# Kernel tuning notes

Measured on AMD Instinct MI355X. Metric: run time of the kernel, lower is better.

Reference implementation:

```python
import jax, jax.numpy as jnp
import numpy as np

B, T, C, H, D = 2, 2048, 1024, 16, 64


def setup_inputs() -> dict:
    key = jax.random.key(0)
    k1, k2, k3, k4, k5 = jax.random.split(key, 5)
    x = jax.random.normal(k1, (B, T, C), dtype=jnp.float32)
    Wq = jax.random.normal(k2, (H, C, D), dtype=jnp.float32) * 0.02
    Wk = jax.random.normal(k3, (H, C, D), dtype=jnp.float32) * 0.02
    Wv = jax.random.normal(k4, (H, C, D), dtype=jnp.float32) * 0.02
    Wo = jax.random.normal(k5, (C, C), dtype=jnp.float32) * 0.02
    bo = jnp.zeros((C,), dtype=jnp.float32)
    return {"x": x, "Wq": Wq, "Wk": Wk, "Wv": Wv, "Wo": Wo, "bo": bo}


def reference(x, Wq, Wk, Wv, Wo, bo):
    # per-head projections (batched over heads instead of a python loop)
    q = jnp.einsum('btc,hcd->bhtd', x, Wq)
    k = jnp.einsum('btc,hcd->bhtd', x, Wk)
    v = jnp.einsum('btc,hcd->bhtd', x, Wv)
    scale = jnp.asarray(D, x.dtype) ** -0.5
    wei = jnp.einsum('bhtd,bhsd->bhts', q, k) * scale  # [B,H,T,T]
    causal = jnp.tril(jnp.ones((T, T), dtype=bool))
    wei = jnp.where(causal, wei, jnp.asarray(-jnp.inf, wei.dtype))
    attn = jax.nn.softmax(wei, axis=-1)
    out = jnp.einsum('bhts,bhsd->bhtd', attn, v)  # [B,H,T,D]
    # concat heads (head order h0..hH-1 along feature dim)
    out = out.transpose(0, 2, 1, 3).reshape(B, T, C)
    # output projection: nn.Linear -> y = x @ W^T + b  (dropout p=0 is identity)
    return out @ Wo.T + bo
```

## Files before the change

### kernel.cpp

```cpp
#include <hip/hip_runtime.h>
#include <hip/hip_bf16.h>
#include <cstdint>
#include <math.h>

#define B_DIM 2
#define T_SEQ 2048
#define C_DIM 1024
#define H_NUM 16
#define D_HEAD 64
#define M_ROWS (B_DIM * T_SEQ)
#define N_QKV (3 * H_NUM * D_HEAD)

using short8  = __attribute__((ext_vector_type(8))) short;
using short4v = __attribute__((ext_vector_type(4))) short;
using f32x4   = __attribute__((ext_vector_type(4))) float;

__device__ __forceinline__ short f2bf(float f) {
  union { __hip_bfloat16 h; short s; } u;
  u.h = __float2bfloat16(f);
  return u.s;
}

__device__ __forceinline__ unsigned pk2bf(float a, float b) {
  union { float f; unsigned u; } ua, ub;
  ua.f = a; ub.f = b;
  return __builtin_amdgcn_perm(ub.u, ua.u, 0x07060302u);
}

__device__ __forceinline__ void gld_lds16(short* lds, const short* g) {
  __builtin_amdgcn_global_load_lds(
      (const unsigned int __attribute__((address_space(1)))*)g,
      (unsigned int __attribute__((address_space(3)))*)lds, 16, 0, 0);
}

#define BAR_VM(N)                                                    \
  do {                                                               \
    asm volatile("s_waitcnt vmcnt(" #N ") lgkmcnt(0)" ::: "memory"); \
    __builtin_amdgcn_s_barrier();                                    \
    __builtin_amdgcn_sched_barrier(0);                               \
  } while (0)

__global__ __launch_bounds__(256) void prep(const float* __restrict__ x,
                                            const float* __restrict__ Wo,
                                            const float* __restrict__ Wq,
                                            const float* __restrict__ Wk,
                                            const float* __restrict__ Wv,
                                            short* __restrict__ xb,
                                            short* __restrict__ Wob,
                                            short* __restrict__ Wt) {
  int bid = blockIdx.x;
  int tid = threadIdx.x;
  if (bid < 2560) {
    const float* in = (bid < 2048) ? x : Wo;
    short* out      = (bid < 2048) ? xb : Wob;
    int i = ((bid < 2048) ? bid : (bid - 2048)) * 256 + tid;
    const float4* p = reinterpret_cast<const float4*>(in) + (size_t)i * 2;
    float4 a = p[0], b = p[1];
    short8 o;
    o[0] = f2bf(a.x); o[1] = f2bf(a.y); o[2] = f2bf(a.z); o[3] = f2bf(a.w);
    o[4] = f2bf(b.x); o[5] = f2bf(b.y); o[6] = f2bf(b.z); o[7] = f2bf(b.w);
    reinterpret_cast<short8*>(out)[i] = o;
    return;
  }
  int pid  = bid - 2560;
  int proj = pid >> 8;
  int h    = (pid >> 4) & 15;
  int cb   = pid & 15;
  const float* W = (proj == 0) ? Wq : ((proj == 1) ? Wk : Wv);
  const float* src = W + ((size_t)h * C_DIM + (size_t)cb * 64) * D_HEAD;

  __shared__ float tile[64][65];
#pragma unroll
  for (int j = 0; j < 4; j++) {
    int flat = tid + j * 256;
    int c    = flat >> 4;
    int d4   = flat & 15;
    float4 v = reinterpret_cast<const float4*>(src + (size_t)c * D_HEAD)[d4];
    tile[c][d4 * 4 + 0] = v.x;
    tile[c][d4 * 4 + 1] = v.y;
    tile[c][d4 * 4 + 2] = v.z;
    tile[c][d4 * 4 + 3] = v.w;
  }
  __syncthreads();

  int d     = tid >> 2;
  int cpart = (tid & 3) * 16;
  short* dst = Wt + ((size_t)(proj * H_NUM + h) * D_HEAD + d) * C_DIM + cb * 64 + cpart;
  short8 o0, o1;
#pragma unroll
  for (int j = 0; j < 8; j++) {
    o0[j] = f2bf(tile[cpart + j][d]);
    o1[j] = f2bf(tile[cpart + 8 + j][d]);
  }
  *reinterpret_cast<short8*>(dst)     = o0;
  *reinterpret_cast<short8*>(dst + 8) = o1;
}

template <int MODE, int BMT>
__global__ __launch_bounds__(256) void gemm_bt(
    const short* __restrict__ A, const short* __restrict__ Bt,
    const float* __restrict__ bias,
    short* __restrict__ qb, short* __restrict__ kb, short* __restrict__ vtb,
    float* __restrict__ outb,
    int M, int N, int K) {
  constexpr int BK = 32;
  constexpr int MR = BMT / 32;
  constexpr int NLA = BMT / 64;
  __shared__ short GL[3 * (BMT + 128) * BK];
  short* Asb = GL;
  short* Bsb = GL + 3 * BMT * BK;

  int tid  = threadIdx.x;
  int lane = tid & 63;
  int wv   = tid >> 6;
  int q15  = lane & 15, g = lane >> 4;
  int ntn  = N >> 7;
  int bpx  = (M / BMT) >> 3;
  int xcd  = blockIdx.x & 7;
  int idx  = blockIdx.x >> 3;
  int bn   = idx / bpx;
  int bm   = xcd * bpx + (idx - bn * bpx);
  int row0 = bm * BMT, col0 = bn << 7;
  int wm   = (wv >> 1) * (BMT / 2);
  int wn   = (wv & 1) << 6;

  f32x4 acc[MR][4];
#pragma unroll
  for (int i = 0; i < MR; i++)
#pragma unroll
    for (int j = 0; j < 4; j++) acc[i][j] = (f32x4){0.f, 0.f, 0.f, 0.f};

  int srccol = ((tid & 3) ^ ((tid >> 3) & 3)) * 8;
  const short* ag = A  + (size_t)(row0 + (tid >> 2)) * K + srccol;
  const short* bg = Bt + (size_t)(col0 + (tid >> 2)) * K + srccol;
  const size_t gstep = (size_t)64 * K;

  auto stage = [&](int ks, int buf) {
    const short* a  = ag + (size_t)ks * BK;
    const short* bb = bg + (size_t)ks * BK;
    gld_lds16(Asb + buf * BMT * BK + tid * 8, a);
    if constexpr (NLA == 2)
      gld_lds16(Asb + buf * BMT * BK + 64 * BK + tid * 8, a + gstep);
    gld_lds16(Bsb + buf * 128 * BK + tid * 8, bb);
    gld_lds16(Bsb + buf * 128 * BK + 64 * BK + tid * 8, bb + gstep);
  };

  int nk = K / BK;
  stage(0, 0);
  stage(1, 1);
  if constexpr (NLA == 2) {
    asm volatile("s_waitcnt vmcnt(4)" ::: "memory");
  } else {
    asm volatile("s_waitcnt vmcnt(3)" ::: "memory");
  }
  __builtin_amdgcn_s_barrier();
  __builtin_amdgcn_sched_barrier(0);

  int rpos = (g ^ ((q15 >> 1) & 3)) * 8;

  for (int k = 0; k < nk; ++k) {
    int buf = k % 3;
    if (k + 2 < nk) stage(k + 2, (k + 2) % 3);

    short8 af[MR], bf[4];
#pragma unroll
    for (int mi = 0; mi < MR; mi++)
      af[mi] = *reinterpret_cast<const short8*>(
          &Asb[buf * BMT * BK + (wm + mi * 16 + q15) * BK + rpos]);
#pragma unroll
    for (int ni = 0; ni < 4; ni++)
      bf[ni] = *reinterpret_cast<const short8*>(
          &Bsb[buf * 128 * BK + (wn + ni * 16 + q15) * BK + rpos]);
#pragma unroll
    for (int mi = 0; mi < MR; mi++)
#pragma unroll
      for (int ni = 0; ni < 4; ni++)
        acc[mi][ni] = __builtin_amdgcn_mfma_f32_16x16x32_bf16(af[mi], bf[ni],
                                                              acc[mi][ni], 0, 0, 0);

    if (k + 1 < nk) {
      if (k + 2 < nk) {
        if constexpr (NLA == 2) { BAR_VM(4); } else { BAR_VM(3); }
      } else {
        BAR_VM(0);
      }
    }
  }

  if constexpr (MODE == 0) {
    constexpr int LDT = 136;
    int proj  = col0 >> 10;
    int b     = row0 >> 11;
    int trow0 = row0 & (T_SEQ - 1);
    int h0    = (col0 >> 6) & 15;
    __syncthreads();
    if (proj < 2) {
      float scl = (proj == 0) ? 0.125f * 1.44269504f : 1.0f;
#pragma unroll
      for (int mi = 0; mi < MR; mi++)
#pragma unroll
        for (int ni = 0; ni < 4; ni++) {
          int t0 = wm + mi * 16 + (g << 2);
          int d2 = wn + ni * 16 + q15;
#pragma unroll
          for (int r = 0; r < 4; r++)
            GL[(t0 + r) * LDT + d2] = f2bf(acc[mi][ni][r] * scl);
        }
      __syncthreads();
      short* dstb = (proj == 0) ? qb : kb;
#pragma unroll
      for (int ps = 0; ps < 8; ps++) {
        int trow  = ps * 16 + (tid >> 4);
        int chunk = tid & 15;
        int hh    = h0 + (chunk >> 3);
        int d     = (chunk & 7) * 8;
        short8 v = *reinterpret_cast<const short8*>(&GL[trow * LDT + chunk * 8]);
        *reinterpret_cast<short8*>(
            dstb + ((size_t)(b * H_NUM + hh) * T_SEQ + trow0 + trow) * D_HEAD + d) = v;
      }
    } else {
#pragma unroll
      for (int mi = 0; mi < MR; mi++)
#pragma unroll
        for (int ni = 0; ni < 4; ni++) {
          int t0 = wm + mi * 16 + (g << 2);
          int d2 = wn + ni * 16 + q15;
          short4v pk;
#pragma unroll
          for (int r = 0; r < 4; r++) pk[r] = f2bf(acc[mi][ni][r]);
          *reinterpret_cast<short4v*>(&GL[d2 * LDT + t0]) = pk;
        }
      __syncthreads();
#pragma unroll
      for (int ps = 0; ps < 8; ps++) {
        int drow  = ps * 16 + (tid >> 4);
        int chunk = tid & 15;
        int hh    = h0 + (drow >> 6);
        int d     = drow & 63;
        short8 v = *reinterpret_cast<const short8*>(&GL[drow * LDT + chunk * 8]);
        *reinterpret_cast<short8*>(
            vtb + ((size_t)(b * H_NUM + hh) * D_HEAD + d) * T_SEQ + trow0 +
            chunk * 8) = v;
      }
    }
  } else {
#pragma unroll
    for (int mi = 0; mi < MR; mi++) {
#pragma unroll
      for (int ni = 0; ni < 4; ni++) {
        int rb  = row0 + wm + mi * 16 + (g << 2);
        int col = col0 + wn + ni * 16 + q15;
        f32x4 v = acc[mi][ni];
        float bb = bias[col];
#pragma unroll
        for (int r = 0; r < 4; r++)
          outb[(size_t)(rb + r) * N + col] = v[r] + bb;
      }
    }
  }
}

__global__ __launch_bounds__(256, 4) void attn_fwd(const short* __restrict__ qg,
                                                   const short* __restrict__ kg,
                                                   const short* __restrict__ vt,
                                                   short* __restrict__ ob) {
  int bid  = blockIdx.x;
  int q2   = bid >> 8;
  int r    = bid & 255;
  int bh   = (r & 7) * 4 + q2;
  int sb   = r >> 3;
  int strip = (q2 & 1) ? sb : 31 - sb;
  int b    = bh >> 4;
  int h    = bh & 15;
  int tid  = threadIdx.x, lane = tid & 63, wv = tid >> 6;
  int q15  = lane & 15, g = lane >> 4;
  int qr   = strip * 64 + wv * 16;

  __shared__ short arena[16384];

  const short* qp = qg + (size_t)bh * T_SEQ * D_HEAD;
  const short* kp = kg + (size_t)bh * T_SEQ * D_HEAD;
  const short* vp = vt + (size_t)bh * D_HEAD * T_SEQ;

  int r8    = lane >> 3;
  int gcb   = ((lane & 7) * 16) ^ (r8 << 4);
  int srow0 = wv * 16;

  int hh = (q15 & 7) << 4;
  int koff0 = ((0 * 64 + g * 16) ^ hh) >> 1;
  int koff1 = ((1 * 64 + g * 16) ^ hh) >> 1;
  int voff[4];
#pragma unroll
  for (int st = 0; st < 4; st++) voff[st] = ((st * 32 + g * 8) ^ hh) >> 1;

  short8 qf[2];
#pragma unroll
  for (int kk = 0; kk < 2; kk++)
    qf[kk] = *reinterpret_cast<const short8*>(
        qp + (size_t)(qr + q15) * D_HEAD + kk * 32 + g * 8);

  f32x4 acc[4];
#pragma unroll
  for (int dt = 0; dt < 4; dt++) acc[dt] = (f32x4){0.f, 0.f, 0.f, 0.f};
  f32x4 lacc = (f32x4){0.f, 0.f, 0.f, 0.f};
  float m_ = -1e30f;

  const short4v ones4 = (short4v){(short)0x3F80, (short)0x3F80,
                                  (short)0x3F80, (short)0x3F80};

  int nch = strip + 1;

  auto stage = [&](int c, int pbuf) {
    const short* ks = kp + (size_t)(c * 64 + srow0 + r8) * D_HEAD + (gcb >> 1);
    const short* vs = vp + (size_t)(srow0 + r8) * T_SEQ + c * 64 + (gcb >> 1);
    short* kd = arena + pbuf * 4096 + srow0 * 64 + lane * 8;
    short* vd = arena + 8192 + pbuf * 4096 + srow0 * 64 + lane * 8;
    gld_lds16(kd, ks);
    gld_lds16(kd + 8 * 64, ks + (size_t)8 * D_HEAD);
    gld_lds16(vd, vs);
    gld_lds16(vd + 8 * 64, vs + (size_t)8 * T_SEQ);
  };

  stage(0, 0);
  BAR_VM(0);

  for (int c = 0; c < nch; ++c) {
    int s0 = c * 64;
    if (c + 1 < nch) stage(c + 1, (c + 1) & 1);
    const short* Kb = arena + (c & 1) * 4096;
    const short* Vb = arena + 8192 + (c & 1) * 4096;

    short8 kf[4][2];
#pragma unroll
    for (int st = 0; st < 4; st++) {
      int rbase = (st * 16 + q15) * 64;
      kf[st][0] = *reinterpret_cast<const short8*>(&Kb[rbase + koff0]);
      kf[st][1] = *reinterpret_cast<const short8*>(&Kb[rbase + koff1]);
    }

    f32x4 sv[4];
#pragma unroll
    for (int st = 0; st < 4; st++) {
      f32x4 s = (f32x4){0.f, 0.f, 0.f, 0.f};
      s = __builtin_amdgcn_mfma_f32_16x16x32_bf16(kf[st][0], qf[0], s, 0, 0, 0);
      s = __builtin_amdgcn_mfma_f32_16x16x32_bf16(kf[st][1], qf[1], s, 0, 0, 0);
      sv[st] = s;
    }

    short4v vf[4][4];
#pragma unroll
    for (int st = 0; st < 4; st++)
#pragma unroll
      for (int dt = 0; dt < 4; dt++)
        vf[st][dt] = *reinterpret_cast<const short4v*>(
            &Vb[(dt * 16 + q15) * 64 + voff[st]]);

    if (c == nch - 1) {
#pragma unroll
      for (int st = 0; st < 4; st++)
#pragma unroll
        for (int r2 = 0; r2 < 4; r2++) {
          int sg = s0 + st * 16 + g * 4 + r2;
          if (sg > qr + q15) sv[st][r2] = -1e30f;
        }
    }

    float t0 = fmaxf(fmaxf(sv[0][0], sv[0][1]), sv[0][2]);
    float t1 = fmaxf(fmaxf(sv[0][3], sv[1][0]), sv[1][1]);
    float t2 = fmaxf(fmaxf(sv[1][2], sv[1][3]), sv[2][0]);
    float t3 = fmaxf(fmaxf(sv[2][1], sv[2][2]), sv[2][3]);
    float t4 = fmaxf(fmaxf(sv[3][0], sv[3][1]), sv[3][2]);
    float mx = fmaxf(fmaxf(fmaxf(t0, t1), t2),
                     fmaxf(fmaxf(t3, t4), sv[3][3]));
    mx = fmaxf(mx, __shfl_xor(mx, 16));
    mx = fmaxf(mx, __shfl_xor(mx, 32));

    if (!__all(mx <= m_ + 11.5f)) {
      float mnew = fmaxf(m_, mx);
      float sc   = __builtin_amdgcn_exp2f(m_ - mnew);
      m_ = mnew;
      lacc *= sc;
#pragma unroll
      for (int dt = 0; dt < 4; dt++) acc[dt] *= sc;
    }
    float mcur = m_;

    short4v pbf[4];
#pragma unroll
    for (int st = 0; st < 4; st++) {
      float p0 = __builtin_amdgcn_exp2f(sv[st][0] - mcur);
      float p1 = __builtin_amdgcn_exp2f(sv[st][1] - mcur);
      float p2 = __builtin_amdgcn_exp2f(sv[st][2] - mcur);
      float p3 = __builtin_amdgcn_exp2f(sv[st][3] - mcur);
      union { short4v s; unsigned u[2]; } P;
      P.u[0] = pk2bf(p0, p1);
      P.u[1] = pk2bf(p2, p3);
      pbf[st] = P.s;
    }

#pragma unroll
    for (int st = 0; st < 4; st++) {
#if __has_builtin(__builtin_amdgcn_mfma_f32_16x16x16bf16_1k)
      lacc = __builtin_amdgcn_mfma_f32_16x16x16bf16_1k(ones4, pbf[st], lacc, 0, 0, 0);
#pragma unroll
      for (int dt = 0; dt < 4; dt++)
        acc[dt] = __builtin_amdgcn_mfma_f32_16x16x16bf16_1k(
            vf[st][dt], pbf[st], acc[dt], 0, 0, 0);
#else
      short4v p4 = pbf[st];
      short8 bz = (short8){p4[0], p4[1], p4[2], p4[3], 0, 0, 0, 0};
      short8 oz = (short8){(short)0x3F80, (short)0x3F80, (short)0x3F80,
                           (short)0x3F80, 0, 0, 0, 0};
      lacc = __builtin_amdgcn_mfma_f32_16x16x32_bf16(oz, bz, lacc, 0, 0, 0);
#pragma unroll
      for (int dt = 0; dt < 4; dt++) {
        short4v v4 = vf[st][dt];
        short8 az = (short8){v4[0], v4[1], v4[2], v4[3], 0, 0, 0, 0};
        acc[dt] =
            __builtin_amdgcn_mfma_f32_16x16x32_bf16(az, bz, acc[dt], 0, 0, 0);
      }
#endif
    }

    BAR_VM(0);
  }

  short* OlW = arena + wv * (16 * 68);
  float inv = 1.0f / lacc[0];
#pragma unroll
  for (int dt = 0; dt < 4; dt++)
#pragma unroll
    for (int r2 = 0; r2 < 4; r2++)
      OlW[q15 * 68 + dt * 16 + g * 4 + r2] = f2bf(acc[dt][r2] * inv);
  int row = lane >> 2, cb = (lane & 3) * 16;
  size_t base = ((size_t)(b * T_SEQ) + qr + row) * C_DIM + h * 64 + cb;
  const short* src = OlW + row * 68 + cb;
  *reinterpret_cast<short8*>(ob + base) = *reinterpret_cast<const short8*>(src);
  *reinterpret_cast<short8*>(ob + base + 8) =
      *reinterpret_cast<const short8*>(src + 8);
}

extern "C" void kernel_launch(void* const* d_in, const int* in_sizes, int n_in,
                              void* d_out, int out_size, void* d_ws, size_t ws_size,
                              hipStream_t stream) {
  const float* x  = (const float*)d_in[0];
  const float* Wq = (const float*)d_in[1];
  const float* Wk = (const float*)d_in[2];
  const float* Wv = (const float*)d_in[3];
  const float* Wo = (const float*)d_in[4];
  const float* bo = (const float*)d_in[5];
  float* out = (float*)d_out;

  char* ws = (char*)d_ws;
  short* xb   = (short*)(ws + 0);
  short* Wt   = (short*)(ws + 8388608);
  short* Wob  = (short*)(ws + 14680064);
  short* qb   = (short*)(ws + 16777216);
  short* kb   = (short*)(ws + 25165824);
  short* vtb  = (short*)(ws + 33554432);
  short* obuf = xb;

  prep<<<3328, 256, 0, stream>>>(x, Wo, Wq, Wk, Wv, xb, Wob, Wt);

  gemm_bt<0, 128><<<(M_ROWS / 128) * (N_QKV / 128), 256, 0, stream>>>(
      xb, Wt, nullptr, qb, kb, vtb, nullptr, M_ROWS, N_QKV, C_DIM);

  attn_fwd<<<1024, 256, 0, stream>>>(qb, kb, vtb, obuf);

  gemm_bt<1, 64><<<(M_ROWS / 64) * (C_DIM / 128), 256, 0, stream>>>(
      obuf, Wob, bo, nullptr, nullptr, nullptr, out, M_ROWS, C_DIM, C_DIM);
}
```

Baseline: 101.7 us.

## Shrink QKV GEMM tile to 64 rows and switch to double-buffered LDS pipeline

Halves the M tile of the QKV projection GEMM, doubling the block count, and replaces the three-stage LDS ring with two buffers that wait for all loads each iteration. The epilogue is generalized to arbitrary BMT with a separately sized shared buffer for the Q/K and V transposes. The goal is more parallelism and occupancy through less LDS per block. In exchange, each block reuses less data per tile and the deeper prefetch is lost, so global load latency may be exposed.

Result: slower. 112.0 us (+10.2%).

```diff
diff --git a/kernel.cpp b/kernel.cpp
--- a/kernel.cpp
+++ b/kernel.cpp
@@ -103,12 +103,15 @@
     short* __restrict__ qb, short* __restrict__ kb, short* __restrict__ vtb,
     float* __restrict__ outb,
     int M, int N, int K) {
-  constexpr int BK = 32;
-  constexpr int MR = BMT / 32;
+  constexpr int BK  = 32;
+  constexpr int MR  = BMT / 32;
   constexpr int NLA = BMT / 64;
-  __shared__ short GL[3 * (BMT + 128) * BK];
-  short* Asb = GL;
-  short* Bsb = GL + 3 * BMT * BK;
+  constexpr int STG = (BMT + 128) * BK;
+  constexpr int EPQ = BMT * 136;
+  constexpr int EPV = 128 * (BMT + 8);
+  constexpr int GL2 = (2 * STG > EPQ) ? (2 * STG) : EPQ;
+  constexpr int GLSZ = (GL2 > EPV) ? GL2 : EPV;
+  __shared__ short GL[GLSZ];
 
   int tid  = threadIdx.x;
   int lane = tid & 63;
@@ -136,59 +139,50 @@
   const size_t gstep = (size_t)64 * K;
 
   auto stage = [&](int ks, int buf) {
+    short* base = GL + buf * STG;
     const short* a  = ag + (size_t)ks * BK;
     const short* bb = bg + (size_t)ks * BK;
-    gld_lds16(Asb + buf * BMT * BK + tid * 8, a);
+    gld_lds16(base + tid * 8, a);
     if constexpr (NLA == 2)
-      gld_lds16(Asb + buf * BMT * BK + 64 * BK + tid * 8, a + gstep);
-    gld_lds16(Bsb + buf * 128 * BK + tid * 8, bb);
-    gld_lds16(Bsb + buf * 128 * BK + 64 * BK + tid * 8, bb + gstep);
+      gld_lds16(base + 64 * BK + tid * 8, a + gstep);
+    gld_lds16(base + BMT * BK + tid * 8, bb);
+    gld_lds16(base + BMT * BK + 64 * BK + tid * 8, bb + gstep);
   };
 
   int nk = K / BK;
   stage(0, 0);
-  stage(1, 1);
-  if constexpr (NLA == 2) {
-    asm volatile("s_waitcnt vmcnt(4)" ::: "memory");
-  } else {
-    asm volatile("s_waitcnt vmcnt(3)" ::: "memory");
-  }
-  __builtin_amdgcn_s_barrier();
-  __builtin_amdgcn_sched_barrier(0);
+  BAR_VM(0);
 
   int rpos = (g ^ ((q15 >> 1) & 3)) * 8;
 
   for (int k = 0; k < nk; ++k) {
-    int buf = k % 3;
-    if (k + 2 < nk) stage(k + 2, (k + 2) % 3);
+    if (k + 1 < nk) stage(k + 1, (k + 1) & 1);
+    const short* Ab = GL + (k & 1) * STG;
+    const short* Bb = Ab + BMT * BK;
 
     short8 af[MR], bf[4];
 #pragma unroll
     for (int mi = 0; mi < MR; mi++)
       af[mi] = *reinterpret_cast<const short8*>(
-          &Asb[buf * BMT * BK + (wm + mi * 16 + q15) * BK + rpos]);
+          &Ab[(wm + mi * 16 + q15) * BK + rpos]);
 #pragma unroll
     for (int ni = 0; ni < 4; ni++)
       bf[ni] = *reinterpret_cast<const short8*>(
-          &Bsb[buf * 128 * BK + (wn + ni * 16 + q15) * BK + rpos]);
+          &Bb[(wn + ni * 16 + q15) * BK + rpos]);
 #pragma unroll
     for (int mi = 0; mi < MR; mi++)
 #pragma unroll
       for (int ni = 0; ni < 4; ni++)
         acc[mi][ni] = __builtin_amdgcn_mfma_f32_16x16x32_bf16(af[mi], bf[ni],
                                                               acc[mi][ni], 0, 0, 0);
-
-    if (k + 1 < nk) {
-      if (k + 2 < nk) {
-        if constexpr (NLA == 2) { BAR_VM(4); } else { BAR_VM(3); }
-      } else {
-        BAR_VM(0);
-      }
-    }
+    BAR_VM(0);
   }
 
   if constexpr (MODE == 0) {
-    constexpr int LDT = 136;
+    constexpr int LDTQ = 136;
+    constexpr int LDTV = BMT + 8;
+    constexpr int NPS  = BMT / 16;
+    constexpr int CPR  = BMT / 8;
     int proj  = col0 >> 10;
     int b     = row0 >> 11;
     int trow0 = row0 & (T_SEQ - 1);
@@ -204,17 +198,17 @@
           int d2 = wn + ni * 16 + q15;
 #pragma unroll
           for (int r = 0; r < 4; r++)
-            GL[(t0 + r) * LDT + d2] = f2bf(acc[mi][ni][r] * scl);
+            GL[(t0 + r) * LDTQ + d2] = f2bf(acc[mi][ni][r] * scl);
         }
       __syncthreads();
       short* dstb = (proj == 0) ? qb : kb;
 #pragma unroll
-      for (int ps = 0; ps < 8; ps++) {
+      for (int ps = 0; ps < NPS; ps++) {
         int trow  = ps * 16 + (tid >> 4);
         int chunk = tid & 15;
         int hh    = h0 + (chunk >> 3);
         int d     = (chunk & 7) * 8;
-        short8 v = *reinterpret_cast<const short8*>(&GL[trow * LDT + chunk * 8]);
+        short8 v = *reinterpret_cast<const short8*>(&GL[trow * LDTQ + chunk * 8]);
         *reinterpret_cast<short8*>(
             dstb + ((size_t)(b * H_NUM + hh) * T_SEQ + trow0 + trow) * D_HEAD + d) = v;
       }
@@ -228,19 +222,20 @@
           short4v pk;
 #pragma unroll
           for (int r = 0; r < 4; r++) pk[r] = f2bf(acc[mi][ni][r]);
-          *reinterpret_cast<short4v*>(&GL[d2 * LDT + t0]) = pk;
+          *reinterpret_cast<short4v*>(&GL[d2 * LDTV + t0]) = pk;
         }
       __syncthreads();
 #pragma unroll
-      for (int ps = 0; ps < 8; ps++) {
-        int drow  = ps * 16 + (tid >> 4);
-        int chunk = tid & 15;
+      for (int ps = 0; ps < NPS; ps++) {
+        int id2   = ps * 256 + tid;
+        int drow  = id2 / CPR;
+        int ch    = id2 % CPR;
         int hh    = h0 + (drow >> 6);
         int d     = drow & 63;
-        short8 v = *reinterpret_cast<const short8*>(&GL[drow * LDT + chunk * 8]);
+        short8 v = *reinterpret_cast<const short8*>(&GL[drow * LDTV + ch * 8]);
         *reinterpret_cast<short8*>(
             vtb + ((size_t)(b * H_NUM + hh) * D_HEAD + d) * T_SEQ + trow0 +
-            chunk * 8) = v;
+            ch * 8) = v;
       }
     }
   } else {
@@ -462,7 +457,7 @@
 
   prep<<<3328, 256, 0, stream>>>(x, Wo, Wq, Wk, Wv, xb, Wob, Wt);
 
-  gemm_bt<0, 128><<<(M_ROWS / 128) * (N_QKV / 128), 256, 0, stream>>>(
+  gemm_bt<0, 64><<<(M_ROWS / 64) * (N_QKV / 128), 256, 0, stream>>>(
       xb, Wt, nullptr, qb, kb, vtb, nullptr, M_ROWS, N_QKV, C_DIM);
 
   attn_fwd<<<1024, 256, 0, stream>>>(qb, kb, vtb, obuf);
```

## Split long causal attention strips into two KV halves with a combine kernel

Applied to the files above, without the earlier changes.

Splits the 11 longest query strips (21-31) of each head into two KV-range partial blocks, which removes the causal work imbalance. Work units are reordered so heavy blocks are scheduled early. The partial outputs are stored unnormalized in bf16 along with the row max and sum. A new combine kernel merges them with a log-sum-exp rescale. This adds an extra launch, partial-buffer traffic and a small bf16 rounding on the partials, in exchange for a shorter tail and better CU balance.

After: 102.5 us. Within noise of the previous version (+0.8%).

```diff
diff --git a/kernel.cpp b/kernel.cpp
--- a/kernel.cpp
+++ b/kernel.cpp
@@ -19,6 +19,11 @@
   union { __hip_bfloat16 h; short s; } u;
   u.h = __float2bfloat16(f);
   return u.s;
+}
+__device__ __forceinline__ float bf2f(short s) {
+  union { unsigned u; float f; } v;
+  v.u = ((unsigned)(unsigned short)s) << 16;
+  return v.f;
 }
 
 __device__ __forceinline__ unsigned pk2bf(float a, float b) {
@@ -263,13 +268,18 @@
 __global__ __launch_bounds__(256, 4) void attn_fwd(const short* __restrict__ qg,
                                                    const short* __restrict__ kg,
                                                    const short* __restrict__ vt,
-                                                   short* __restrict__ ob) {
+                                                   short* __restrict__ ob,
+                                                   short* __restrict__ Pp,
+                                                   float* __restrict__ mlp) {
   int bid  = blockIdx.x;
-  int q2   = bid >> 8;
-  int r    = bid & 255;
-  int bh   = (r & 7) * 4 + q2;
-  int sb   = r >> 3;
-  int strip = (q2 & 1) ? sb : 31 - sb;
+  int bh   = (bid & 7) * 4 + ((bid >> 3) & 3);
+  int slot = bid >> 5;
+  int strip, c0, c1, half = 0;
+  bool part;
+  if (slot < 5)       { strip = 20 - slot;  c0 = 0;  c1 = strip + 1; part = false; }
+  else if (slot < 16) { strip = slot + 16;  c0 = 0;  c1 = 16;        part = true;  half = 0; }
+  else if (slot < 27) { strip = 47 - slot;  c0 = 16; c1 = strip + 1; part = true;  half = 1; }
+  else                { strip = 42 - slot;  c0 = 0;  c1 = strip + 1; part = false; }
   int b    = bh >> 4;
   int h    = bh & 15;
   int tid  = threadIdx.x, lane = tid & 63, wv = tid >> 6;
@@ -307,8 +317,6 @@
 
   const short4v ones4 = (short4v){(short)0x3F80, (short)0x3F80,
                                   (short)0x3F80, (short)0x3F80};
-
-  int nch = strip + 1;
 
   auto stage = [&](int c, int pbuf) {
     const short* ks = kp + (size_t)(c * 64 + srow0 + r8) * D_HEAD + (gcb >> 1);
@@ -321,12 +329,12 @@
     gld_lds16(vd + 8 * 64, vs + (size_t)8 * T_SEQ);
   };
 
-  stage(0, 0);
+  stage(c0, c0 & 1);
   BAR_VM(0);
 
-  for (int c = 0; c < nch; ++c) {
+  for (int c = c0; c < c1; ++c) {
     int s0 = c * 64;
-    if (c + 1 < nch) stage(c + 1, (c + 1) & 1);
+    if (c + 1 < c1) stage(c + 1, (c + 1) & 1);
     const short* Kb = arena + (c & 1) * 4096;
     const short* Vb = arena + 8192 + (c & 1) * 4096;
 
@@ -355,7 +363,7 @@
         vf[st][dt] = *reinterpret_cast<const short4v*>(
             &Vb[(dt * 16 + q15) * 64 + voff[st]]);
 
-    if (c == nch - 1) {
+    if (c == strip) {
 #pragma unroll
       for (int st = 0; st < 4; st++)
 #pragma unroll
@@ -426,18 +434,78 @@
   }
 
   short* OlW = arena + wv * (16 * 68);
-  float inv = 1.0f / lacc[0];
-#pragma unroll
-  for (int dt = 0; dt < 4; dt++)
-#pragma unroll
-    for (int r2 = 0; r2 < 4; r2++)
-      OlW[q15 * 68 + dt * 16 + g * 4 + r2] = f2bf(acc[dt][r2] * inv);
-  int row = lane >> 2, cb = (lane & 3) * 16;
-  size_t base = ((size_t)(b * T_SEQ) + qr + row) * C_DIM + h * 64 + cb;
-  const short* src = OlW + row * 68 + cb;
-  *reinterpret_cast<short8*>(ob + base) = *reinterpret_cast<const short8*>(src);
-  *reinterpret_cast<short8*>(ob + base + 8) =
-      *reinterpret_cast<const short8*>(src + 8);
+  if (!part) {
+    float inv = 1.0f / lacc[0];
+#pragma unroll
+    for (int dt = 0; dt < 4; dt++)
+#pragma unroll
+      for (int r2 = 0; r2 < 4; r2++)
+        OlW[q15 * 68 + dt * 16 + g * 4 + r2] = f2bf(acc[dt][r2] * inv);
+    int row = lane >> 2, cb = (lane & 3) * 16;
+    size_t base = ((size_t)(b * T_SEQ) + qr + row) * C_DIM + h * 64 + cb;
+    const short* src = OlW + row * 68 + cb;
+    *reinterpret_cast<short8*>(ob + base) = *reinterpret_cast<const short8*>(src);
+    *reinterpret_cast<short8*>(ob + base + 8) =
+        *reinterpret_cast<const short8*>(src + 8);
+  } else {
+#pragma unroll
+    for (int dt = 0; dt < 4; dt++)
+#pragma unroll
+      for (int r2 = 0; r2 < 4; r2++)
+        OlW[q15 * 68 + dt * 16 + g * 4 + r2] = f2bf(acc[dt][r2]);
+    int si = strip - 21;
+    int row = lane >> 2, cb = (lane & 3) * 16;
+    size_t pbase = ((size_t)(bh * 11 + si) * 2 + half) * 4096 +
+                   (wv * 16 + row) * 64 + cb;
+    const short* src = OlW + row * 68 + cb;
+    *reinterpret_cast<short8*>(Pp + pbase) =
+        *reinterpret_cast<const short8*>(src);
+    *reinterpret_cast<short8*>(Pp + pbase + 8) =
+        *reinterpret_cast<const short8*>(src + 8);
+    if (lane < 16) {
+      float* mlr = mlp + ((size_t)((bh * 11 + si) * 2 + half)) * 128 +
+                   (wv * 16 + lane) * 2;
+      mlr[0] = m_;
+      mlr[1] = lacc[0];
+    }
+  }
+}
+
+__global__ __launch_bounds__(256) void combine(const short* __restrict__ Pp,
+                                               const float* __restrict__ mlp,
+                                               short* __restrict__ ob) {
+  int bid = blockIdx.x;
+  int bh  = bid / 11, si = bid % 11;
+  int strip = si + 21;
+  int b = bh >> 4, h = bh & 15;
+  int t = threadIdx.x;
+  int lr = t >> 2, dg = (t & 3) * 16;
+
+  size_t mbase = ((size_t)(bh * 11 + si) * 2) * 128 + lr * 2;
+  float m0 = mlp[mbase], l0 = mlp[mbase + 1];
+  float m1 = mlp[mbase + 128], l1 = mlp[mbase + 129];
+  float m  = fmaxf(m0, m1);
+  float w0 = __builtin_amdgcn_exp2f(m0 - m);
+  float w1 = __builtin_amdgcn_exp2f(m1 - m);
+  float inv = 1.0f / (l0 * w0 + l1 * w1);
+  w0 *= inv;
+  w1 *= inv;
+
+  const short* P0 = Pp + ((size_t)(bh * 11 + si) * 2) * 4096 + lr * 64 + dg;
+  const short* P1 = P0 + 4096;
+  short8 a0 = *reinterpret_cast<const short8*>(P0);
+  short8 a1 = *reinterpret_cast<const short8*>(P0 + 8);
+  short8 c0 = *reinterpret_cast<const short8*>(P1);
+  short8 c1 = *reinterpret_cast<const short8*>(P1 + 8);
+  short8 o0, o1;
+#pragma unroll
+  for (int j = 0; j < 8; j++) {
+    o0[j] = f2bf(bf2f(a0[j]) * w0 + bf2f(c0[j]) * w1);
+    o1[j] = f2bf(bf2f(a1[j]) * w0 + bf2f(c1[j]) * w1);
+  }
+  short* dst = ob + ((size_t)(b * T_SEQ) + strip * 64 + lr) * C_DIM + h * 64 + dg;
+  *reinterpret_cast<short8*>(dst)     = o0;
+  *reinterpret_cast<short8*>(dst + 8) = o1;
 }
 
 extern "C" void kernel_launch(void* const* d_in, const int* in_sizes, int n_in,
@@ -459,13 +527,16 @@
   short* kb   = (short*)(ws + 25165824);
   short* vtb  = (short*)(ws + 33554432);
   short* obuf = xb;
+  short* Pp   = Wt;
+  float* mlp  = (float*)(ws + 8388608 + 5767168);
 
   prep<<<3328, 256, 0, stream>>>(x, Wo, Wq, Wk, Wv, xb, Wob, Wt);
 
   gemm_bt<0, 128><<<(M_ROWS / 128) * (N_QKV / 128), 256, 0, stream>>>(
       xb, Wt, nullptr, qb, kb, vtb, nullptr, M_ROWS, N_QKV, C_DIM);
 
-  attn_fwd<<<1024, 256, 0, stream>>>(qb, kb, vtb, obuf);
+  attn_fwd<<<1376, 256, 0, stream>>>(qb, kb, vtb, obuf, Pp, mlp);
+  combine<<<352, 256, 0, stream>>>(Pp, mlp, obuf);
 
   gemm_bt<1, 64><<<(M_ROWS / 64) * (C_DIM / 128), 256, 0, stream>>>(
       obuf, Wob, bo, nullptr, nullptr, nullptr, out, M_ROWS, C_DIM, C_DIM);
```
